# Optimization experiments

Hardware: AMD Instinct MI355X
Metric: run time of the kernel (lower is better)

## Reference

```python
import jax, jax.numpy as jnp
import numpy as np

INPUT_SIZE = 2048
REDUCED = 128
HIDDEN = 32


def setup_inputs() -> dict:
    key = jax.random.key(0)
    ks = jax.random.split(key, 12)
    N, T, S = 32, 1024, 8
    x = jax.random.normal(ks[0], (N, S, 768), dtype=jnp.float32)
    fea = jax.random.normal(ks[1], (N, T, INPUT_SIZE), dtype=jnp.float32)
    fea_len = jax.random.randint(ks[2], (N,), 0, T - S).astype(jnp.int64)
    s_ann = 1.0 / np.sqrt(INPUT_SIZE)
    s_rnn = 1.0 / np.sqrt(HIDDEN)
    s_q = 1.0 / np.sqrt(HIDDEN)
    W_ann = jax.random.uniform(ks[3], (REDUCED, INPUT_SIZE), minval=-s_ann, maxval=s_ann)
    b_ann = jax.random.uniform(ks[4], (REDUCED,), minval=-s_ann, maxval=s_ann)
    W_ih = jax.random.uniform(ks[5], (3 * HIDDEN, REDUCED), minval=-s_rnn, maxval=s_rnn)
    W_hh = jax.random.uniform(ks[6], (3 * HIDDEN, HIDDEN), minval=-s_rnn, maxval=s_rnn)
    b_ih = jax.random.uniform(ks[7], (3 * HIDDEN,), minval=-s_rnn, maxval=s_rnn)
    b_hh = jax.random.uniform(ks[8], (3 * HIDDEN,), minval=-s_rnn, maxval=s_rnn)
    W_q = jax.random.uniform(ks[9], (1, HIDDEN), minval=-s_q, maxval=s_q)
    b_q = jax.random.uniform(ks[10], (1,), minval=-s_q, maxval=s_q)
    return {"x": x, "fea": fea, "fea_len": fea_len, "W_ann": W_ann, "b_ann": b_ann,
            "W_ih": W_ih, "W_hh": W_hh, "b_ih": b_ih, "b_hh": b_hh,
            "W_q": W_q, "b_q": b_q}


def _gru(gx, W_hh, b_hh, h0):
    # gx: (T, N, 3H) precomputed input projections; torch gate order: r, z, n
    def step(h, gxt):
        gh = h @ W_hh.T + b_hh
        xr, xz, xn = jnp.split(gxt, 3, axis=-1)
        hr, hz, hn = jnp.split(gh, 3, axis=-1)
        r = jax.nn.sigmoid(xr + hr)
        z = jax.nn.sigmoid(xz + hz)
        n = jnp.tanh(xn + r * hn)
        h_new = (1.0 - z) * n + z * h
        return h_new, h_new
    _, hs = jax.lax.scan(step, h0, gx)
    return hs  # (T, N, H)


def reference(x, fea, fea_len, W_ann, b_ann, W_ih, W_hh, b_ih, b_hh, W_q, b_q):
    N, T, _ = fea.shape
    f = fea @ W_ann.T + b_ann                    # (N, T, 128)
    gx = f @ W_ih.T + b_ih                       # (N, T, 3H)
    h0 = jnp.zeros((N, HIDDEN), dtype=f.dtype)
    hs = _gru(jnp.swapaxes(gx, 0, 1), W_hh, b_hh, h0)   # (T, N, H)
    outputs = jnp.swapaxes(hs, 0, 1)             # (N, T, H)
    q = (outputs @ W_q.T + b_q)[..., 0]          # (N, T)
    # vectorized masked segment-mean replacing the per-sample python loop
    L = fea_len + x.shape[1]                     # (N,)
    mask = jnp.arange(T)[None, :] < L[:, None]   # (N, T)
    score = jnp.sum(q * mask, axis=1) / L.astype(q.dtype)
    return score
```

## Files before the change

kernel.cpp:

```cpp
#include <hip/hip_runtime.h>
#include <hip/hip_bf16.h>
#include <math.h>

#define NS   32
#define TS   1024
#define KIN  2048
#define RED  128
#define HID  32
#define G3   96
#define SEQ  8

#define GX_FLOATS (NS * TS * G3)
#define W_ELEMS   (G3 * KIN)

typedef __attribute__((ext_vector_type(8))) short  short8;
typedef __attribute__((ext_vector_type(4))) float  floatx4;
typedef __attribute__((ext_vector_type(2))) float  floatx2;
typedef __attribute__((ext_vector_type(2))) unsigned int uint2v;

__device__ __forceinline__ int load_len(const int* __restrict__ p, int n) {
    bool is64 = (p[1] == 0) && (p[3] == 0) && (p[5] == 0) && (p[7] == 0);
    if (is64) return (int)((const long long*)p)[n];
    return p[n];
}

__device__ __forceinline__ unsigned short f2bf(float x) {
    unsigned u = __float_as_uint(x);
    unsigned r = u + 0x7fffu + ((u >> 16) & 1u);
    return (unsigned short)(r >> 16);
}
__device__ __forceinline__ float bfu2f(unsigned short u) {
    return __uint_as_float(((unsigned)u) << 16);
}

__device__ __forceinline__ float fexp2(float x) {
#if __has_builtin(__builtin_amdgcn_exp2f)
    return __builtin_amdgcn_exp2f(x);
#else
    return exp2f(x);
#endif
}

__device__ __forceinline__ void swap16(unsigned& a, unsigned& b) {
#if __has_builtin(__builtin_amdgcn_permlane16_swap)
    uint2v r = __builtin_amdgcn_permlane16_swap(a, b, false, false);
    a = r.x; b = r.y;
#else
    asm("v_permlane16_swap_b32 %0, %1" : "+v"(a), "+v"(b));
#endif
}
__device__ __forceinline__ void swap32(unsigned& a, unsigned& b) {
#if __has_builtin(__builtin_amdgcn_permlane32_swap)
    uint2v r = __builtin_amdgcn_permlane32_swap(a, b, false, false);
    a = r.x; b = r.y;
#else
    asm("v_permlane32_swap_b32 %0, %1" : "+v"(a), "+v"(b));
#endif
}

__device__ __forceinline__ float xor32sum(float x) {
    unsigned a = __float_as_uint(x), b = a;
    swap32(a, b);
    return __uint_as_float(a) + __uint_as_float(b);
}

#define DPPM(srcv, ctrl) __uint_as_float((unsigned)__builtin_amdgcn_update_dpp( \
        (int)__float_as_uint(srcv), (int)__float_as_uint(srcv), (ctrl), 0xF, 0xF, false))

__device__ __forceinline__ void cvt_hilo(const float* f, short8& hi, short8& lo) {
    #pragma unroll
    for (int p = 0; p < 4; ++p) {
        float2 fv = make_float2(f[2*p], f[2*p+1]);
        union { __hip_bfloat162 b2; unsigned short us[2]; } H, L;
        H.b2 = __float22bfloat162_rn(fv);
        float2 hb = __bfloat1622float2(H.b2);
        L.b2 = __float22bfloat162_rn(make_float2(fv.x - hb.x, fv.y - hb.y));
        hi[2*p] = (short)H.us[0]; hi[2*p+1] = (short)H.us[1];
        lo[2*p] = (short)L.us[0]; lo[2*p+1] = (short)L.us[1];
    }
}

__global__ __launch_bounds__(256) void k_prep(
        const float* __restrict__ W_ann, const float* __restrict__ b_ann,
        const float* __restrict__ W_ih,  const float* __restrict__ b_ih,
        unsigned short* __restrict__ Whi, unsigned short* __restrict__ Wlo,
        float* __restrict__ b_comb) {
    if (blockIdx.x == 768) {
        int j = threadIdx.x;
        if (j < G3) {
            float acc = b_ih[j];
            #pragma unroll 8
            for (int m = 0; m < RED; ++m) acc += W_ih[j * RED + m] * b_ann[m];
            b_comb[j] = acc;
        }
        return;
    }
    int id = blockIdx.x * 256 + threadIdx.x;
    int j = id >> 11;
    int k = id & (KIN - 1);
    float acc = 0.0f;
    #pragma unroll 8
    for (int m = 0; m < RED; ++m) acc += W_ih[j * RED + m] * W_ann[m * KIN + k];
    unsigned short h = f2bf(acc);
    Whi[id] = h;
    Wlo[id] = f2bf(acc - bfu2f(h));
}

__global__ __launch_bounds__(256) void k_gemm(
        const float* __restrict__ fea, const int* __restrict__ flen,
        const unsigned short* __restrict__ Whi,
        const unsigned short* __restrict__ Wlo,
        const float* __restrict__ b_comb,
        float* __restrict__ gx) {
    const int n  = blockIdx.x;
    const int t0 = blockIdx.y * 128;
    const int L  = load_len(flen, n) + SEQ;
    if (t0 >= L) return;

    const int tid  = threadIdx.x;
    const int w    = tid >> 6;
    const int ln   = tid & 63;
    const int mr   = ln & 15;
    const int quad = ln >> 4;

    const size_t arow0 = ((size_t)(n * TS + t0 + w * 32 + mr)) * KIN + quad * 8;
    const size_t arow1 = arow0 + (size_t)16 * KIN;
    int boff[6];
    #pragma unroll
    for (int nf = 0; nf < 6; ++nf) boff[nf] = (nf * 16 + mr) * KIN + quad * 8;

    floatx4 acc[2][6];
    #pragma unroll
    for (int mf = 0; mf < 2; ++mf)
        #pragma unroll
        for (int nf = 0; nf < 6; ++nf) acc[mf][nf] = (floatx4){0.f, 0.f, 0.f, 0.f};

    #pragma unroll 1
    for (int c = 0; c < KIN / 64; ++c) {
        #pragma unroll
        for (int ks = 0; ks < 2; ++ks) {
            const int ko = c * 64 + ks * 32;
            float fa[8], fb[8];
            {
                float4 a0 = *(const float4*)(fea + arow0 + ko);
                float4 a1 = *(const float4*)(fea + arow0 + ko + 4);
                float4 b0 = *(const float4*)(fea + arow1 + ko);
                float4 b1 = *(const float4*)(fea + arow1 + ko + 4);
                fa[0]=a0.x; fa[1]=a0.y; fa[2]=a0.z; fa[3]=a0.w;
                fa[4]=a1.x; fa[5]=a1.y; fa[6]=a1.z; fa[7]=a1.w;
                fb[0]=b0.x; fb[1]=b0.y; fb[2]=b0.z; fb[3]=b0.w;
                fb[4]=b1.x; fb[5]=b1.y; fb[6]=b1.z; fb[7]=b1.w;
            }
            short8 ah0, al0, ah1, al1;
            cvt_hilo(fa, ah0, al0);
            cvt_hilo(fb, ah1, al1);
            #pragma unroll
            for (int nf = 0; nf < 6; ++nf) {
                short8 bh = *(const short8*)(Whi + boff[nf] + ko);
                short8 bl = *(const short8*)(Wlo + boff[nf] + ko);
                acc[0][nf] = __builtin_amdgcn_mfma_f32_16x16x32_bf16(ah0, bh, acc[0][nf], 0, 0, 0);
                acc[0][nf] = __builtin_amdgcn_mfma_f32_16x16x32_bf16(ah0, bl, acc[0][nf], 0, 0, 0);
                acc[0][nf] = __builtin_amdgcn_mfma_f32_16x16x32_bf16(al0, bh, acc[0][nf], 0, 0, 0);
                acc[1][nf] = __builtin_amdgcn_mfma_f32_16x16x32_bf16(ah1, bh, acc[1][nf], 0, 0, 0);
                acc[1][nf] = __builtin_amdgcn_mfma_f32_16x16x32_bf16(ah1, bl, acc[1][nf], 0, 0, 0);
                acc[1][nf] = __builtin_amdgcn_mfma_f32_16x16x32_bf16(al1, bh, acc[1][nf], 0, 0, 0);
            }
        }
    }

    #pragma unroll
    for (int mf = 0; mf < 2; ++mf) {
        const int tbase = t0 + w * 32 + mf * 16 + quad * 4;
        #pragma unroll
        for (int nf = 0; nf < 6; ++nf) {
            const float bc = b_comb[nf * 16 + mr];
            float* gp = gx + ((size_t)(n * TS + tbase)) * G3 + nf * 16 + mr;
            #pragma unroll
            for (int r = 0; r < 4; ++r)
                gp[(size_t)r * G3] = acc[mf][nf][r] + bc;
        }
    }
}

__global__ __launch_bounds__(64)
__attribute__((amdgpu_waves_per_eu(1, 1)))
void k_scan(
        const float* __restrict__ gx, const int* __restrict__ flen,
        const float* __restrict__ W_hh, const float* __restrict__ b_hh,
        const float* __restrict__ W_q,  const float* __restrict__ b_q,
        float* __restrict__ out) {
    const int n    = blockIdx.x;
    const int lane = threadIdx.x;
    const int j    = lane & 31;
    const int kh   = lane >> 5;
    const int l15  = lane & 15;
    const int L    = load_len(flen, n) + SEQ;

    const float LOG2E = 1.4426950408889634f;

    const int MT[16] = {0,1,2,3, 7,6,5,4, 15,14,13,12, 8,9,10,11};

    floatx2 wr2[8], wz2[8], wn2[8];
    #pragma unroll
    for (int k2 = 0; k2 < 8; ++k2) {
        const int ka = kh * 16 + (l15 ^ MT[2*k2]);
        const int kb = kh * 16 + (l15 ^ MT[2*k2+1]);
        wr2[k2].x = -LOG2E * W_hh[(size_t)(j)      * HID + ka];
        wr2[k2].y = -LOG2E * W_hh[(size_t)(j)      * HID + kb];
        wz2[k2].x = -LOG2E * W_hh[(size_t)(32 + j) * HID + ka];
        wz2[k2].y = -LOG2E * W_hh[(size_t)(32 + j) * HID + kb];
        wn2[k2].x = 2.0f * LOG2E * W_hh[(size_t)(64 + j) * HID + ka];
        wn2[k2].y = 2.0f * LOG2E * W_hh[(size_t)(64 + j) * HID + kb];
    }
    const float mh  = -0.5f * LOG2E;
    const float brm = mh * b_hh[j];
    const float bzm = mh * b_hh[32 + j];
    const float bnm = LOG2E * b_hh[64 + j];
    const float xnf = 2.0f * LOG2E;
    const float wq  = W_q[j];
    const float bq  = b_q[0];
    const bool  hi  = (lane >= 32);

    bool selY;
    {
        unsigned a = (unsigned)lane, b = (unsigned)lane;
        swap16(a, b);
        const bool dirA = ((a & 16u) == 0u);
        selY = dirA ? hi : !hi;
    }

    const float* gbase = gx + (size_t)n * TS * G3;

    float rg[8][3];
    #pragma unroll
    for (int i = 0; i < 8; ++i) {
        const float* p = gbase + (size_t)i * G3;
        rg[i][0] = p[j]; rg[i][1] = p[32 + j]; rg[i][2] = p[64 + j];
    }

    floatx2 hv2[8];
    #pragma unroll
    for (int k2 = 0; k2 < 8; ++k2) hv2[k2] = (floatx2){0.f, 0.f};
    float h = 0.0f, qacc = 0.0f;

    #define GRU_STEP(XR, XZ, XN, DO_UPDATE)                                   \
    {                                                                         \
        floatx2 aA = (floatx2){__builtin_fmaf(mh, (XR), brm), 0.f};           \
        floatx2 zA = (floatx2){__builtin_fmaf(mh, (XZ), bzm), 0.f};           \
        floatx2 nA = (floatx2){bnm, 0.f};                                     \
        floatx2 aB = (floatx2){0.f, 0.f}, zB = aB, nB = aB;                   \
        const float xn2 = xnf * (XN);                                         \
        _Pragma("unroll")                                                     \
        for (int k2 = 0; k2 < 4; ++k2) {                                      \
            aA += wr2[k2] * hv2[k2];   aB += wr2[k2+4] * hv2[k2+4];           \
            zA += wz2[k2] * hv2[k2];   zB += wz2[k2+4] * hv2[k2+4];           \
            nA += wn2[k2] * hv2[k2];   nB += wn2[k2+4] * hv2[k2+4];           \
        }                                                                     \
        floatx2 av = aA + aB, zv = zA + zB, nv = nA + nB;                     \
        float sr   = xor32sum(av.x + av.y);                                   \
        float sz   = xor32sum(zv.x + zv.y);                                   \
        float dnb2 = xor32sum(nv.x + nv.y);                                   \
        float r    = __builtin_amdgcn_rcpf(1.0f + fexp2(sr));                 \
        float z    = __builtin_amdgcn_rcpf(1.0f + fexp2(sz));                 \
        float sn   = __builtin_fmaf(r, dnb2, xn2);                            \
        float u    = __builtin_amdgcn_rcpf(1.0f + fexp2(sn));                 \
        float nng  = __builtin_fmaf(-2.0f, u, 1.0f);                          \
        float hnew = __builtin_fmaf(z, h - nng, nng);                         \
        if (DO_UPDATE) {                                                      \
            h = hnew;                                                         \
            qacc = __builtin_fmaf(wq, hnew, qacc);                            \
        }                                                                     \
        {        \
            unsigned pa = __float_as_uint(h), pb = pa;                        \
            swap16(pa, pb);                                                   \
            hv2[0].x = selY ? __uint_as_float(pb) : __uint_as_float(pa);      \
            hv2[0].y = DPPM(hv2[0].x, 0xB1);                       \
            hv2[1].x = DPPM(hv2[0].x, 0x4E);                       \
            hv2[1].y = DPPM(hv2[0].y, 0x4E);                       \
            hv2[2].x = DPPM(hv2[0].x, 0x141);                      \
            hv2[2].y = DPPM(hv2[0].y, 0x141);                      \
            hv2[3].x = DPPM(hv2[1].x, 0x141);                      \
            hv2[3].y = DPPM(hv2[1].y, 0x141);                      \
            hv2[4].x = DPPM(hv2[0].x, 0x140);                      \
            hv2[4].y = DPPM(hv2[0].y, 0x140);                      \
            hv2[5].x = DPPM(hv2[1].x, 0x140);                      \
            hv2[5].y = DPPM(hv2[1].y, 0x140);                      \
            hv2[6].x = DPPM(hv2[2].x, 0x140);                      \
            hv2[6].y = DPPM(hv2[2].y, 0x140);                      \
            hv2[7].x = DPPM(hv2[3].x, 0x140);                      \
            hv2[7].y = DPPM(hv2[3].y, 0x140);                      \
        }                                                                     \
    }

    const int Lfull = L & ~7;

    for (int tb = 0; tb < Lfull; tb += 8) {
        #pragma unroll
        for (int i = 0; i < 8; ++i) {
            const int t = tb + i;
            const float xr = rg[i][0], xz = rg[i][1], xn = rg[i][2];
            {
                int tl = t + 8; if (tl > TS - 1) tl = TS - 1;
                const float* p = gbase + (size_t)tl * G3;
                rg[i][0] = p[j]; rg[i][1] = p[32 + j]; rg[i][2] = p[64 + j];
            }
            GRU_STEP(xr, xz, xn, true)
        }
    }

    if (Lfull < L) {
        #pragma unroll
        for (int i = 0; i < 8; ++i) {
            const int t = Lfull + i;
            const float xr = rg[i][0], xz = rg[i][1], xn = rg[i][2];
            GRU_STEP(xr, xz, xn, (t < L))
        }
    }
    #undef GRU_STEP

    #pragma unroll
    for (int off = 32; off > 0; off >>= 1) qacc += __shfl_xor(qacc, off, 64);
    if (lane == 0) out[n] = qacc * 0.5f / (float)L + bq;
}

extern "C" void kernel_launch(void* const* d_in, const int* in_sizes, int n_in,
                              void* d_out, int out_size, void* d_ws, size_t ws_size,
                              hipStream_t stream) {
    const float* fea   = (const float*)d_in[1];
    const int*   flen  = (const int*)  d_in[2];
    const float* W_ann = (const float*)d_in[3];
    const float* b_ann = (const float*)d_in[4];
    const float* W_ih  = (const float*)d_in[5];
    const float* W_hh  = (const float*)d_in[6];
    const float* b_ih  = (const float*)d_in[7];
    const float* b_hh  = (const float*)d_in[8];
    const float* W_q   = (const float*)d_in[9];
    const float* b_q   = (const float*)d_in[10];
    float* out = (float*)d_out;

    float*          ws_f   = (float*)d_ws;
    float*          gx     = ws_f;
    unsigned short* Whi    = (unsigned short*)(ws_f + GX_FLOATS);
    unsigned short* Wlo    = Whi + W_ELEMS;
    float*          b_comb = (float*)(Wlo + W_ELEMS);

    k_prep<<<769, 256, 0, stream>>>(W_ann, b_ann, W_ih, b_ih, Whi, Wlo, b_comb);

    dim3 g2(NS, TS / 128);
    k_gemm<<<g2, 256, 0, stream>>>(fea, flen, Whi, Wlo, b_comb, gx);

    k_scan<<<NS, 64, 0, stream>>>(gx, flen, W_hh, b_hh, W_q, b_q, out);
}
```

Before: 664.7 us.

## Fuse GEMM and GRU scan into one persistent kernel with tile-ready counters

Merges the projection GEMM and the recurrent scan into a single launch. Scan blocks consume gx tiles as soon as producer blocks signal completion through per-tile atomic counters, so the sequential scan overlaps the GEMM instead of waiting for it to finish. GEMM work is redistributed to 128 persistent blocks that each loop over time tiles of one sample. This relies on all 136 blocks being co-resident, otherwise the spin-waits can deadlock. It also uses fewer GEMM blocks with smaller per-wave tiles, which may lower GEMM throughput.

```diff
diff --git a/kernel.cpp b/kernel.cpp
--- a/kernel.cpp
+++ b/kernel.cpp
@@ -13,6 +13,10 @@
 #define GX_FLOATS (NS * TS * G3)
 #define W_ELEMS   (G3 * KIN)
 
+#define SCAN_BLOCKS 8
+#define GEMM_BLOCKS 128
+#define STRIPS_PER_TILE 4
+
 typedef __attribute__((ext_vector_type(8))) short  short8;
 typedef __attribute__((ext_vector_type(4))) float  floatx4;
 typedef __attribute__((ext_vector_type(2))) float  floatx2;
@@ -66,6 +70,17 @@
 
 #define DPPM(srcv, ctrl) __uint_as_float((unsigned)__builtin_amdgcn_update_dpp( \
         (int)__float_as_uint(srcv), (int)__float_as_uint(srcv), (ctrl), 0xF, 0xF, false))
+
+__device__ __forceinline__ float aload(const float* p) {
+    return __uint_as_float(__hip_atomic_load((const unsigned*)p,
+            __ATOMIC_RELAXED, __HIP_MEMORY_SCOPE_AGENT));
+}
+__device__ __forceinline__ void wait_tile(const unsigned* c) {
+    while (__hip_atomic_load(c, __ATOMIC_ACQUIRE, __HIP_MEMORY_SCOPE_AGENT)
+           < (unsigned)STRIPS_PER_TILE) {
+        __builtin_amdgcn_s_sleep(2);
+    }
+}
 
 __device__ __forceinline__ void cvt_hilo(const float* f, short8& hi, short8& lo) {
     #pragma unroll
@@ -84,9 +99,10 @@
         const float* __restrict__ W_ann, const float* __restrict__ b_ann,
         const float* __restrict__ W_ih,  const float* __restrict__ b_ih,
         unsigned short* __restrict__ Whi, unsigned short* __restrict__ Wlo,
-        float* __restrict__ b_comb) {
+        float* __restrict__ b_comb, unsigned* __restrict__ cnt) {
     if (blockIdx.x == 768) {
         int j = threadIdx.x;
+        cnt[j] = 0;
         if (j < G3) {
             float acc = b_ih[j];
             #pragma unroll 8
@@ -106,91 +122,90 @@
     Wlo[id] = f2bf(acc - bfu2f(h));
 }
 
-__global__ __launch_bounds__(256) void k_gemm(
+__device__ __forceinline__ void gemm_role(
         const float* __restrict__ fea, const int* __restrict__ flen,
         const unsigned short* __restrict__ Whi,
         const unsigned short* __restrict__ Wlo,
         const float* __restrict__ b_comb,
-        float* __restrict__ gx) {
-    const int n  = blockIdx.x;
-    const int t0 = blockIdx.y * 128;
+        float* __restrict__ gx, unsigned* __restrict__ cnt) {
+    const int b2 = blockIdx.x - SCAN_BLOCKS;
+    const int n  = b2 & 31;
+    const int q  = b2 >> 5;
     const int L  = load_len(flen, n) + SEQ;
-    if (t0 >= L) return;
 
     const int tid  = threadIdx.x;
     const int w    = tid >> 6;
     const int ln   = tid & 63;
     const int mr   = ln & 15;
     const int quad = ln >> 4;
-
-    const size_t arow0 = ((size_t)(n * TS + t0 + w * 32 + mr)) * KIN + quad * 8;
-    const size_t arow1 = arow0 + (size_t)16 * KIN;
-    int boff[6];
-    #pragma unroll
-    for (int nf = 0; nf < 6; ++nf) boff[nf] = (nf * 16 + mr) * KIN + quad * 8;
-
-    floatx4 acc[2][6];
-    #pragma unroll
-    for (int mf = 0; mf < 2; ++mf)
-        #pragma unroll
-        for (int nf = 0; nf < 6; ++nf) acc[mf][nf] = (floatx4){0.f, 0.f, 0.f, 0.f};
-
-    #pragma unroll 1
-    for (int c = 0; c < KIN / 64; ++c) {
-        #pragma unroll
-        for (int ks = 0; ks < 2; ++ks) {
-            const int ko = c * 64 + ks * 32;
-            float fa[8], fb[8];
-            {
-                float4 a0 = *(const float4*)(fea + arow0 + ko);
-                float4 a1 = *(const float4*)(fea + arow0 + ko + 4);
-                float4 b0 = *(const float4*)(fea + arow1 + ko);
-                float4 b1 = *(const float4*)(fea + arow1 + ko + 4);
-                fa[0]=a0.x; fa[1]=a0.y; fa[2]=a0.z; fa[3]=a0.w;
-                fa[4]=a1.x; fa[5]=a1.y; fa[6]=a1.z; fa[7]=a1.w;
-                fb[0]=b0.x; fb[1]=b0.y; fb[2]=b0.z; fb[3]=b0.w;
-                fb[4]=b1.x; fb[5]=b1.y; fb[6]=b1.z; fb[7]=b1.w;
+    const int mf   = w & 1;
+    const int nfb  = (w >> 1) * 3;
+
+    int boff[3];
+    #pragma unroll
+    for (int nf2 = 0; nf2 < 3; ++nf2)
+        boff[nf2] = ((nfb + nf2) * 16 + mr) * KIN + quad * 8;
+
+    for (int ty = 0; ty < 8; ++ty) {
+        const int t0 = ty * 128 + q * 32;
+        if (t0 < L) {
+            const size_t arow =
+                ((size_t)(n * TS + t0 + mf * 16 + mr)) * KIN + quad * 8;
+            floatx4 acc[3];
+            #pragma unroll
+            for (int nf2 = 0; nf2 < 3; ++nf2) acc[nf2] = (floatx4){0.f,0.f,0.f,0.f};
+
+            #pragma unroll 1
+            for (int c = 0; c < KIN / 64; ++c) {
+                #pragma unroll
+                for (int ks = 0; ks < 2; ++ks) {
+                    const int ko = c * 64 + ks * 32;
+                    float fa[8];
+                    {
+                        float4 a0 = *(const float4*)(fea + arow + ko);
+                        float4 a1 = *(const float4*)(fea + arow + ko + 4);
+                        fa[0]=a0.x; fa[1]=a0.y; fa[2]=a0.z; fa[3]=a0.w;
+                        fa[4]=a1.x; fa[5]=a1.y; fa[6]=a1.z; fa[7]=a1.w;
+                    }
+                    short8 ah, al;
+                    cvt_hilo(fa, ah, al);
+                    #pragma unroll
+                    for (int nf2 = 0; nf2 < 3; ++nf2) {
+                        short8 bh = *(const short8*)(Whi + boff[nf2] + ko);
+                        short8 bl = *(const short8*)(Wlo + boff[nf2] + ko);
+                        acc[nf2] = __builtin_amdgcn_mfma_f32_16x16x32_bf16(ah, bh, acc[nf2], 0, 0, 0);
+                        acc[nf2] = __builtin_amdgcn_mfma_f32_16x16x32_bf16(ah, bl, acc[nf2], 0, 0, 0);
+                        acc[nf2] = __builtin_amdgcn_mfma_f32_16x16x32_bf16(al, bh, acc[nf2], 0, 0, 0);
+                    }
+                }
             }
-            short8 ah0, al0, ah1, al1;
-            cvt_hilo(fa, ah0, al0);
-            cvt_hilo(fb, ah1, al1);
+            const int tbase = t0 + mf * 16 + quad * 4;
             #pragma unroll
-            for (int nf = 0; nf < 6; ++nf) {
-                short8 bh = *(const short8*)(Whi + boff[nf] + ko);
-                short8 bl = *(const short8*)(Wlo + boff[nf] + ko);
-                acc[0][nf] = __builtin_amdgcn_mfma_f32_16x16x32_bf16(ah0, bh, acc[0][nf], 0, 0, 0);
-                acc[0][nf] = __builtin_amdgcn_mfma_f32_16x16x32_bf16(ah0, bl, acc[0][nf], 0, 0, 0);
-                acc[0][nf] = __builtin_amdgcn_mfma_f32_16x16x32_bf16(al0, bh, acc[0][nf], 0, 0, 0);
-                acc[1][nf] = __builtin_amdgcn_mfma_f32_16x16x32_bf16(ah1, bh, acc[1][nf], 0, 0, 0);
-                acc[1][nf] = __builtin_amdgcn_mfma_f32_16x16x32_bf16(ah1, bl, acc[1][nf], 0, 0, 0);
-                acc[1][nf] = __builtin_amdgcn_mfma_f32_16x16x32_bf16(al1, bh, acc[1][nf], 0, 0, 0);
+            for (int nf2 = 0; nf2 < 3; ++nf2) {
+                const float bc = b_comb[(nfb + nf2) * 16 + mr];
+                float* gp = gx + ((size_t)(n * TS + tbase)) * G3 + (nfb + nf2) * 16 + mr;
+                #pragma unroll
+                for (int r = 0; r < 4; ++r)
+                    gp[(size_t)r * G3] = acc[nf2][r] + bc;
             }
         }
-    }
-
-    #pragma unroll
-    for (int mf = 0; mf < 2; ++mf) {
-        const int tbase = t0 + w * 32 + mf * 16 + quad * 4;
-        #pragma unroll
-        for (int nf = 0; nf < 6; ++nf) {
-            const float bc = b_comb[nf * 16 + mr];
-            float* gp = gx + ((size_t)(n * TS + tbase)) * G3 + nf * 16 + mr;
-            #pragma unroll
-            for (int r = 0; r < 4; ++r)
-                gp[(size_t)r * G3] = acc[mf][nf][r] + bc;
-        }
-    }
-}
-
-__global__ __launch_bounds__(64)
-__attribute__((amdgpu_waves_per_eu(1, 1)))
-void k_scan(
+        __threadfence();
+        __syncthreads();
+        if (tid == 0)
+            __hip_atomic_fetch_add(&cnt[n * 8 + ty], 1u,
+                                   __ATOMIC_RELEASE, __HIP_MEMORY_SCOPE_AGENT);
+    }
+}
+
+__device__ __forceinline__ void scan_role(
         const float* __restrict__ gx, const int* __restrict__ flen,
         const float* __restrict__ W_hh, const float* __restrict__ b_hh,
         const float* __restrict__ W_q,  const float* __restrict__ b_q,
-        float* __restrict__ out) {
-    const int n    = blockIdx.x;
-    const int lane = threadIdx.x;
+        float* __restrict__ out, const unsigned* __restrict__ cnt) {
+    const int tid  = threadIdx.x;
+    const int wv   = tid >> 6;
+    const int lane = tid & 63;
+    const int n    = blockIdx.x * 4 + wv;
     const int j    = lane & 31;
     const int kh   = lane >> 5;
     const int l15  = lane & 15;
@@ -230,12 +245,17 @@
     }
 
     const float* gbase = gx + (size_t)n * TS * G3;
+    const unsigned* cn = cnt + n * 8;
+    const int tclip = (L - 1) >> 7;
+
+    wait_tile(cn + 0);
+    int twait = 0;
 
     float rg[8][3];
     #pragma unroll
     for (int i = 0; i < 8; ++i) {
         const float* p = gbase + (size_t)i * G3;
-        rg[i][0] = p[j]; rg[i][1] = p[32 + j]; rg[i][2] = p[64 + j];
+        rg[i][0] = aload(p + j); rg[i][1] = aload(p + 32 + j); rg[i][2] = aload(p + 64 + j);
     }
 
     floatx2 hv2[8];
@@ -295,6 +315,10 @@
     const int Lfull = L & ~7;
 
     for (int tb = 0; tb < Lfull; tb += 8) {
+        int tneed = (tb + 15) >> 7;
+        if (tneed > tclip) tneed = tclip;
+        while (twait < tneed) { ++twait; wait_tile(cn + twait); }
+
         #pragma unroll
         for (int i = 0; i < 8; ++i) {
             const int t = tb + i;
@@ -302,7 +326,7 @@
             {
                 int tl = t + 8; if (tl > TS - 1) tl = TS - 1;
                 const float* p = gbase + (size_t)tl * G3;
-                rg[i][0] = p[j]; rg[i][1] = p[32 + j]; rg[i][2] = p[64 + j];
+                rg[i][0] = aload(p + j); rg[i][1] = aload(p + 32 + j); rg[i][2] = aload(p + 64 + j);
             }
             GRU_STEP(xr, xz, xn, true)
         }
@@ -321,6 +345,23 @@
     #pragma unroll
     for (int off = 32; off > 0; off >>= 1) qacc += __shfl_xor(qacc, off, 64);
     if (lane == 0) out[n] = qacc * 0.5f / (float)L + bq;
+}
+
+__global__ __launch_bounds__(256)
+__attribute__((amdgpu_waves_per_eu(1, 2)))
+void k_fused(
+        const float* __restrict__ fea, const int* __restrict__ flen,
+        const unsigned short* __restrict__ Whi,
+        const unsigned short* __restrict__ Wlo,
+        const float* __restrict__ b_comb, float* __restrict__ gx,
+        const float* __restrict__ W_hh, const float* __restrict__ b_hh,
+        const float* __restrict__ W_q,  const float* __restrict__ b_q,
+        float* __restrict__ out, unsigned* __restrict__ cnt) {
+    if (blockIdx.x >= SCAN_BLOCKS) {
+        gemm_role(fea, flen, Whi, Wlo, b_comb, gx, cnt);
+    } else {
+        scan_role(gx, flen, W_hh, b_hh, W_q, b_q, out, cnt);
+    }
 }
 
 extern "C" void kernel_launch(void* const* d_in, const int* in_sizes, int n_in,
@@ -343,11 +384,10 @@
     unsigned short* Whi    = (unsigned short*)(ws_f + GX_FLOATS);
     unsigned short* Wlo    = Whi + W_ELEMS;
     float*          b_comb = (float*)(Wlo + W_ELEMS);
-
-    k_prep<<<769, 256, 0, stream>>>(W_ann, b_ann, W_ih, b_ih, Whi, Wlo, b_comb);
-
-    dim3 g2(NS, TS / 128);
-    k_gemm<<<g2, 256, 0, stream>>>(fea, flen, Whi, Wlo, b_comb, gx);
-
-    k_scan<<<NS, 64, 0, stream>>>(gx, flen, W_hh, b_hh, W_q, b_q, out);
-}
+    unsigned*       cnt    = (unsigned*)(b_comb + G3);
+
+    k_prep<<<769, 256, 0, stream>>>(W_ann, b_ann, W_ih, b_ih, Whi, Wlo, b_comb, cnt);
+
+    k_fused<<<SCAN_BLOCKS + GEMM_BLOCKS, 256, 0, stream>>>(
+        fea, flen, Whi, Wlo, b_comb, gx, W_hh, b_hh, W_q, b_q, out, cnt);
+}
```

After: 1.028 ms. 1.55x slower.
